# Performance work log

Measured on AMD Instinct MI355X. Metric: run time of the kernel, lower is better.

Reference implementation:

```python
import jax, jax.numpy as jnp
import numpy as np

N_TOTAL = 524288  # total entity embeddings in flat ragged buffer
A = 262144        # number of actors
D = 256           # d_model
C = 32            # n_choice


def setup_inputs() -> dict:
    key = jax.random.key(0)
    k1, k2, k3, k4, k5 = jax.random.split(key, 5)
    x_data = jax.random.normal(k1, (N_TOTAL, D), dtype=jnp.float32)
    W = jax.random.normal(k2, (C, D), dtype=jnp.float32) * 0.01  # layer_init std=0.01
    b = jnp.zeros((C,), dtype=jnp.float32)
    actors = jax.random.randint(k3, (A,), 0, N_TOTAL, dtype=jnp.int64)
    mask = jax.random.randint(k4, (A, C), 0, 2, dtype=jnp.int32)
    mask = mask.at[:, 0].set(1)  # guarantee at least one valid choice per actor
    pa = jax.random.randint(k5, (A,), 0, C, dtype=jnp.int64)
    # prev_actions must be valid under the mask (as a real rollout would be)
    valid = jnp.take_along_axis(mask, pa[:, None], axis=1).squeeze(-1)
    prev_actions = jnp.where(valid != 0, pa, 0)
    return {"x_data": x_data, "W": W, "b": b, "actors": actors,
            "mask": mask, "prev_actions": prev_actions}


def reference(x_data, W, b, actors, mask, prev_actions):
    # gather actor embeddings: [A, D]
    actor_embeds = x_data[actors]
    # linear projection: [A, C]
    logits = jnp.einsum('ad,cd->ac', actor_embeds, W) + b
    # masked fill with -inf where mask == 0
    logits = jnp.where(mask == 0, -jnp.inf, logits)
    # Categorical: normalized logits = log_softmax
    logp = jax.nn.log_softmax(logits, axis=-1)
    p = jnp.exp(logp)
    action = prev_actions  # prev_actions provided -> no sampling
    logprob = jnp.take_along_axis(logp, action[:, None], axis=1).squeeze(-1)
    # entropy: -sum p*logp over valid entries (0*(-inf) -> 0)
    entropy = -jnp.sum(jnp.where(mask != 0, p * logp, 0.0), axis=-1)
    return action, logprob, entropy, logp
```

## Files before the change

kernel.cpp:

```cpp
#include <hip/hip_runtime.h>
#include <math.h>


constexpr int A_TOTAL = 262144;
constexpr int DMODEL  = 256;
constexpr int NCHOICE = 32;
constexpr int APW     = 32;
constexpr int APB     = 128;
constexpr int PADC    = 36;

#define MASK_NEG 1.0e30f

#define DPP_SUM_STEP(x, ctrl)                                              \
    (x) += __int_as_float(__builtin_amdgcn_update_dpp(                     \
        0, __float_as_int(x), (ctrl), 0xf, 0xf, true))
#define DPP_MAX_STEP(x, ctrl)                                              \
    (x) = fmaxf((x), __int_as_float(__builtin_amdgcn_update_dpp(           \
        0, __float_as_int(x), (ctrl), 0xf, 0xf, true)))

#define DPP_REDUCE_DG(x)                                                   \
    do { DPP_SUM_STEP(x, 0xB1); DPP_SUM_STEP(x, 0x4E);                     \
         DPP_SUM_STEP(x, 0x128); DPP_SUM_STEP(x, 0x124); } while (0)
#define DPP_RED8_SUM(x)                                                    \
    do { DPP_SUM_STEP(x, 0xB1); DPP_SUM_STEP(x, 0x4E);                     \
         DPP_SUM_STEP(x, 0x141); } while (0)
#define DPP_RED8_MAX(x)                                                    \
    do { DPP_MAX_STEP(x, 0xB1); DPP_MAX_STEP(x, 0x4E);                     \
         DPP_MAX_STEP(x, 0x141); } while (0)

__global__ __launch_bounds__(256, 2)
void cat_action_head(const float* __restrict__ x_data,
                     const float* __restrict__ W,
                     const float* __restrict__ bvec,
                     const int*   __restrict__ actors,
                     const int*   __restrict__ mask,
                     const int*   __restrict__ prev_actions,
                     float* __restrict__ out)
{
    const int t  = threadIdx.x;
    const int wv = t >> 6;
    const int ln = t & 63;
    const int dg = ln & 15;
    const int cg = ln >> 4;
    const int q  = ln & 7;
    const int ar = ln >> 3;

    float* out_action  = out;
    float* out_logprob = out + A_TOTAL;
    float* out_entropy = out + 2 * A_TOTAL;
    float* out_logp    = out + 3 * A_TOTAL;

    __shared__ float part[4][8][PADC];

    const int wbase = (blockIdx.x * 4 + wv) * APW;

    float4 Wf[8][4];
#pragma unroll
    for (int k = 0; k < 8; ++k) {
        const float* Wr = W + (size_t)(cg * 8 + k) * DMODEL + dg * 4;
#pragma unroll
        for (int j = 0; j < 4; ++j)
            Wf[k][j] = *reinterpret_cast<const float4*>(Wr + j * 64);
    }

    const float4 bq = *reinterpret_cast<const float4*>(&bvec[q * 4]);

    int4 mvC = *reinterpret_cast<const int4*>(
                   &mask[(size_t)(wbase + ar) * NCHOICE + q * 4]);
    int  pvC = prev_actions[wbase + ar];

#define AIDX(I) __builtin_amdgcn_readfirstlane(actors[wbase + (I)])

#define LOADX(DST, I)                                                      \
    do {                                                                   \
        const float* xb_ = x_data + (size_t)AIDX(I) * DMODEL + dg * 4;     \
        DST[0] = *reinterpret_cast<const float4*>(xb_);                    \
        DST[1] = *reinterpret_cast<const float4*>(xb_ + 64);               \
        DST[2] = *reinterpret_cast<const float4*>(xb_ + 128);              \
        DST[3] = *reinterpret_cast<const float4*>(xb_ + 192);              \
    } while (0)

#define COMP(XV, II)                                                       \
    do {                                                                   \
        float acc_[8] = {0.f,0.f,0.f,0.f,0.f,0.f,0.f,0.f};                 \
        _Pragma("unroll")                                                  \
        for (int j = 0; j < 4; ++j) {                                      \
            _Pragma("unroll")                                              \
            for (int k2 = 0; k2 < 8; ++k2) {                               \
                acc_[k2] = fmaf(XV[j].x, Wf[k2][j].x, acc_[k2]);           \
                acc_[k2] = fmaf(XV[j].y, Wf[k2][j].y, acc_[k2]);           \
                acc_[k2] = fmaf(XV[j].z, Wf[k2][j].z, acc_[k2]);           \
                acc_[k2] = fmaf(XV[j].w, Wf[k2][j].w, acc_[k2]);           \
            }                                                              \
        }                                                                  \
        _Pragma("unroll")                                                  \
        for (int k2 = 0; k2 < 8; ++k2) DPP_REDUCE_DG(acc_[k2]);            \
        if (dg == 0) {                                                     \
            float4 v0_; v0_.x=acc_[0]; v0_.y=acc_[1];                      \
                        v0_.z=acc_[2]; v0_.w=acc_[3];                      \
            float4 v1_; v1_.x=acc_[4]; v1_.y=acc_[5];                      \
                        v1_.z=acc_[6]; v1_.w=acc_[7];                      \
            *reinterpret_cast<float4*>(&part[wv][II][cg * 8])     = v0_;   \
            *reinterpret_cast<float4*>(&part[wv][II][cg * 8 + 4]) = v1_;   \
        }                                                                  \
    } while (0)

#define EPI(K, MV, PV)                                                     \
    do {                                                                   \
        const int aep_ = wbase + (K) * 8 + ar;                             \
        const float4 pv4_ =                                                \
            *reinterpret_cast<const float4*>(&part[wv][ar][q * 4]);        \
        const float lg0 = (MV).x ? pv4_.x + bq.x : -MASK_NEG;              \
        const float lg1 = (MV).y ? pv4_.y + bq.y : -MASK_NEG;              \
        const float lg2 = (MV).z ? pv4_.z + bq.z : -MASK_NEG;              \
        const float lg3 = (MV).w ? pv4_.w + bq.w : -MASK_NEG;              \
        float mx = fmaxf(fmaxf(lg0, lg1), fmaxf(lg2, lg3));                \
        DPP_RED8_MAX(mx);                                                  \
        const float e0 = expf(lg0 - mx);                                   \
        const float e1 = expf(lg1 - mx);                                   \
        const float e2 = expf(lg2 - mx);                                   \
        const float e3 = expf(lg3 - mx);                                   \
        float se = (e0 + e1) + (e2 + e3);                                  \
        DPP_RED8_SUM(se);                                                  \
        const float lse = mx + logf(se);                                   \
        const float rse = 1.0f / se;                                       \
        const float lp0 = lg0 - lse;                                       \
        const float lp1 = lg1 - lse;                                       \
        const float lp2 = lg2 - lse;                                       \
        const float lp3 = lg3 - lse;                                       \
        float4 lpv; lpv.x=lp0; lpv.y=lp1; lpv.z=lp2; lpv.w=lp3;            \
        *reinterpret_cast<float4*>(                                        \
            &out_logp[(size_t)aep_ * NCHOICE + q * 4]) = lpv;              \
        float ent = fmaf(e0, lp0, fmaf(e1, lp1, fmaf(e2, lp2, e3 * lp3))); \
        DPP_RED8_SUM(ent);                                                 \
        float sel = ((PV) == q * 4 + 0) ? lp0 : 0.0f;                      \
        sel = ((PV) == q * 4 + 1) ? lp1 : sel;                             \
        sel = ((PV) == q * 4 + 2) ? lp2 : sel;                             \
        sel = ((PV) == q * 4 + 3) ? lp3 : sel;                             \
        DPP_RED8_SUM(sel);                                                 \
        if (q == 0) {                                                      \
            out_logprob[aep_] = sel;                                       \
            out_entropy[aep_] = -ent * rse;                                \
            out_action[aep_]  = (float)(PV);                               \
        }                                                                  \
    } while (0)

#define CHUNK(C)                                                           \
    do {                                                                   \
        float4 xva[4], xvb[4], xvc[4];                                     \
        LOADX(xva, (C) * 8 + 0);                                           \
        LOADX(xvb, (C) * 8 + 1);                                           \
        LOADX(xvc, (C) * 8 + 2);                                           \
        COMP(xva, 0); LOADX(xva, (C) * 8 + 3);                             \
        COMP(xvb, 1); LOADX(xvb, (C) * 8 + 4);                             \
        COMP(xvc, 2); LOADX(xvc, (C) * 8 + 5);                             \
        COMP(xva, 3); LOADX(xva, (C) * 8 + 6);                             \
        COMP(xvb, 4); LOADX(xvb, (C) * 8 + 7);                             \
        COMP(xvc, 5);                                                      \
        COMP(xva, 6);                                                      \
        COMP(xvb, 7);                                                      \
        int4 mvN_;                                                         \
        int  pvN_ = 0;                                                     \
        if ((C) < 3) {                                                     \
            mvN_ = *reinterpret_cast<const int4*>(                         \
                &mask[(size_t)(wbase + ((C) + 1) * 8 + ar) * NCHOICE       \
                      + q * 4]);                                           \
            pvN_ = prev_actions[wbase + ((C) + 1) * 8 + ar];               \
        }                                                                  \
        EPI(C, mvC, pvC);                                                  \
        if ((C) < 3) { mvC = mvN_; pvC = pvN_; }                           \
    } while (0)

    CHUNK(0);
    CHUNK(1);
    CHUNK(2);
    CHUNK(3);

#undef CHUNK
#undef EPI
#undef COMP
#undef LOADX
#undef AIDX
}

extern "C" void kernel_launch(void* const* d_in, const int* in_sizes, int n_in,
                              void* d_out, int out_size, void* d_ws, size_t ws_size,
                              hipStream_t stream)
{
    const float* x_data = (const float*)d_in[0];
    const float* W      = (const float*)d_in[1];
    const float* bvec   = (const float*)d_in[2];
    const int*   actors = (const int*)d_in[3];
    const int*   mask   = (const int*)d_in[4];
    const int*   prev   = (const int*)d_in[5];
    float*       o      = (float*)d_out;

    const int nblocks = A_TOTAL / APB;
    cat_action_head<<<nblocks, 256, 0, stream>>>(x_data, W, bvec, actors, mask,
                                                 prev, o);
}
```

Before: 111.8 us.

## Preload actor indices and run a continuous 4-deep gather pipeline across chunks

All 32 actor indices for a wave are now loaded up front with vector int4 loads into scalar registers, so each row gather no longer waits on its own dependent index load. The per-chunk 3-buffer software pipeline is replaced by a continuous 4-buffer rolling pipeline that runs across chunk boundaries, keeping gathers in flight while the epilogues execute. Mask and prev-action loads now happen after each epilogue instead of before it. The extra live buffers raise register pressure and could reduce occupancy.

```diff
diff --git a/kernel.cpp b/kernel.cpp
--- a/kernel.cpp
+++ b/kernel.cpp
@@ -54,6 +54,16 @@
 
     const int wbase = (blockIdx.x * 4 + wv) * APW;
 
+    int sa[APW];
+#pragma unroll
+    for (int v = 0; v < APW / 4; ++v) {
+        const int4 av = *reinterpret_cast<const int4*>(&actors[wbase + v * 4]);
+        sa[v * 4 + 0] = __builtin_amdgcn_readfirstlane(av.x);
+        sa[v * 4 + 1] = __builtin_amdgcn_readfirstlane(av.y);
+        sa[v * 4 + 2] = __builtin_amdgcn_readfirstlane(av.z);
+        sa[v * 4 + 3] = __builtin_amdgcn_readfirstlane(av.w);
+    }
+
     float4 Wf[8][4];
 #pragma unroll
     for (int k = 0; k < 8; ++k) {
@@ -69,11 +79,9 @@
                    &mask[(size_t)(wbase + ar) * NCHOICE + q * 4]);
     int  pvC = prev_actions[wbase + ar];
 
-#define AIDX(I) __builtin_amdgcn_readfirstlane(actors[wbase + (I)])
-
 #define LOADX(DST, I)                                                      \
     do {                                                                   \
-        const float* xb_ = x_data + (size_t)AIDX(I) * DMODEL + dg * 4;     \
+        const float* xb_ = x_data + (size_t)sa[(I)] * DMODEL + dg * 4;     \
         DST[0] = *reinterpret_cast<const float4*>(xb_);                    \
         DST[1] = *reinterpret_cast<const float4*>(xb_ + 64);               \
         DST[2] = *reinterpret_cast<const float4*>(xb_ + 128);              \
@@ -145,42 +153,40 @@
         }                                                                  \
     } while (0)
 
-#define CHUNK(C)                                                           \
-    do {                                                                   \
-        float4 xva[4], xvb[4], xvc[4];                                     \
-        LOADX(xva, (C) * 8 + 0);                                           \
-        LOADX(xvb, (C) * 8 + 1);                                           \
-        LOADX(xvc, (C) * 8 + 2);                                           \
-        COMP(xva, 0); LOADX(xva, (C) * 8 + 3);                             \
-        COMP(xvb, 1); LOADX(xvb, (C) * 8 + 4);                             \
-        COMP(xvc, 2); LOADX(xvc, (C) * 8 + 5);                             \
-        COMP(xva, 3); LOADX(xva, (C) * 8 + 6);                             \
-        COMP(xvb, 4); LOADX(xvb, (C) * 8 + 7);                             \
-        COMP(xvc, 5);                                                      \
-        COMP(xva, 6);                                                      \
-        COMP(xvb, 7);                                                      \
-        int4 mvN_;                                                         \
-        int  pvN_ = 0;                                                     \
-        if ((C) < 3) {                                                     \
-            mvN_ = *reinterpret_cast<const int4*>(                         \
-                &mask[(size_t)(wbase + ((C) + 1) * 8 + ar) * NCHOICE       \
-                      + q * 4]);                                           \
-            pvN_ = prev_actions[wbase + ((C) + 1) * 8 + ar];               \
-        }                                                                  \
-        EPI(C, mvC, pvC);                                                  \
-        if ((C) < 3) { mvC = mvN_; pvC = pvN_; }                           \
-    } while (0)
-
-    CHUNK(0);
-    CHUNK(1);
-    CHUNK(2);
-    CHUNK(3);
-
-#undef CHUNK
+#define PFM(G)                                                             \
+    do {                                                                   \
+        mvC = *reinterpret_cast<const int4*>(                              \
+            &mask[(size_t)(wbase + (G) * 8 + ar) * NCHOICE + q * 4]);      \
+        pvC = prev_actions[wbase + (G) * 8 + ar];                          \
+    } while (0)
+
+#define STEP(I, B)                                                         \
+    do {                                                                   \
+        COMP(B, (I) & 7);                                                  \
+        if ((I) + 4 < APW) LOADX(B, (I) + 4);                              \
+    } while (0)
+
+    float4 X0[4], X1[4], X2[4], X3[4];
+    LOADX(X0, 0); LOADX(X1, 1); LOADX(X2, 2); LOADX(X3, 3);
+
+    STEP(0, X0);  STEP(1, X1);  STEP(2, X2);  STEP(3, X3);
+    STEP(4, X0);  STEP(5, X1);  STEP(6, X2);  STEP(7, X3);
+    EPI(0, mvC, pvC); PFM(1);
+    STEP(8, X0);  STEP(9, X1);  STEP(10, X2); STEP(11, X3);
+    STEP(12, X0); STEP(13, X1); STEP(14, X2); STEP(15, X3);
+    EPI(1, mvC, pvC); PFM(2);
+    STEP(16, X0); STEP(17, X1); STEP(18, X2); STEP(19, X3);
+    STEP(20, X0); STEP(21, X1); STEP(22, X2); STEP(23, X3);
+    EPI(2, mvC, pvC); PFM(3);
+    STEP(24, X0); STEP(25, X1); STEP(26, X2); STEP(27, X3);
+    STEP(28, X0); STEP(29, X1); STEP(30, X2); STEP(31, X3);
+    EPI(3, mvC, pvC);
+
+#undef STEP
+#undef PFM
 #undef EPI
 #undef COMP
 #undef LOADX
-#undef AIDX
 }
 
 extern "C" void kernel_launch(void* const* d_in, const int* in_sizes, int n_in,
```

Result: faster. 92.95 us (-16.9%).
